# Kernel optimization log

Hardware: AMD Instinct MI355X
Metric: run time of the kernel (lower is better)

## Reference

```python
import jax, jax.numpy as jnp
import numpy as np

DIM = 192
HEADS = 6
WS = (6, 12)          # (lat, lon) window
INPUT_SHAPE = (186, 360)
TOW = INPUT_SHAPE[0] // WS[0]   # 31 latitude window types
N_WIN = WS[0] * WS[1]           # 72 tokens per window


def _position_index():
    """Earth-specific relative-position index (static, numpy)."""
    ws0, ws1 = WS
    coords_hi = np.arange(ws0)
    coords_hj = -np.arange(ws0) * ws0
    coords_w = np.arange(ws1)
    c1 = np.stack(np.meshgrid(coords_hi, coords_w, indexing='ij'))  # (2, ws0, ws1)
    c2 = np.stack(np.meshgrid(coords_hj, coords_w, indexing='ij'))
    f1 = c1.reshape(2, -1)
    f2 = c2.reshape(2, -1)
    coords = f1[:, :, None] - f2[:, None, :]      # (2, N, N)
    coords = coords.transpose(1, 2, 0).copy()     # (N, N, 2)
    coords[:, :, 1] += ws1 - 1                    # shift lon diff to >= 0
    coords[:, :, 0] *= 2 * ws1 - 1                # row stride in bias table
    return jnp.asarray(coords.sum(-1).reshape(-1))  # (N*N,) int


def setup_inputs() -> dict:
    key = jax.random.key(0)
    ks = jax.random.split(key, 6)
    B = 2
    nW = INPUT_SHAPE[1] // WS[1]          # 30
    B_ = B * TOW * nW                     # 1860
    table_rows = (2 * WS[1] - 1) * WS[0] * WS[0]  # 828
    return {
        "x": jax.random.normal(ks[0], (B_, N_WIN, DIM), dtype=jnp.float32),
        "mask": jnp.zeros((nW, N_WIN, N_WIN), dtype=jnp.float32),
        "w_qkv": jax.random.normal(ks[1], (DIM, 3 * DIM), dtype=jnp.float32) * 0.02,
        "b_qkv": jnp.zeros((3 * DIM,), dtype=jnp.float32),
        "w_out": jax.random.normal(ks[2], (DIM, DIM), dtype=jnp.float32) * 0.02,
        "b_out": jnp.zeros((DIM,), dtype=jnp.float32),
        "bias_table": jax.random.normal(ks[3], (table_rows, TOW, HEADS), dtype=jnp.float32) * 0.02,
    }


def reference(x, mask, w_qkv, b_qkv, w_out, b_out, bias_table):
    B_, N, dim = x.shape
    hd = dim // HEADS
    scale = hd ** -0.5
    # fused QKV projection
    qkv = (x @ w_qkv + b_qkv).reshape(B_, N, 3, HEADS, hd)
    qkv = qkv.transpose(2, 0, 3, 1, 4)            # (3, B_, H, N, hd)
    q, k, v = qkv[0] * scale, qkv[1], qkv[2]
    attn = jnp.einsum('bhnd,bhmd->bhnm', q, k)    # (B_, H, N, N)
    # earth-specific bias: gather table rows by relative-position index,
    # tiled across the window batch exactly as the torch code's .repeat()
    rep = B_ // TOW
    pos = _position_index()                       # (N*N,)
    bias = bias_table[jnp.tile(pos, rep)]         # (rep*N*N, TOW, H)
    bias = bias.reshape(N, N, -1, HEADS).transpose(2, 3, 0, 1)  # (B_, H, N, N)
    attn = attn + bias
    # window mask (broadcast over groups of nW lon-windows)
    nW = mask.shape[0]
    attn = attn.reshape(B_ // nW, nW, HEADS, N, N) + mask[None, :, None]
    attn = attn.reshape(B_, HEADS, N, N)
    attn = jax.nn.softmax(attn, axis=-1)          # dropout is identity (p=0 / eval)
    out = jnp.einsum('bhnm,bhmd->bhnd', attn, v)  # (B_, H, N, hd)
    out = out.transpose(0, 2, 1, 3).reshape(B_, N, dim)
    return out @ w_out + b_out
```

## Files before the change

### kernel.cpp

```cpp
#include <hip/hip_runtime.h>
#include <cstddef>

typedef short bf16x8 __attribute__((ext_vector_type(8)));
typedef float f32x4  __attribute__((ext_vector_type(4)));

namespace {
constexpr float QSCALE = 0.17677669529663687f;

constexpr size_t BQKV_OFF = 0;
constexpr size_t WOUT_OFF = 576 * 384 * 2;
constexpr size_t BQG_OFF  = WOUT_OFF + 192 * 384 * 2;
constexpr size_t QG_OFF   = BQG_OFF + 576 * 4;
constexpr size_t KG_OFF   = QG_OFF + (size_t)11160 * 2304 * 2;
constexpr size_t VG_OFF   = KG_OFF + (size_t)11160 * 2304 * 2;

constexpr int AXS = 392;
}

__device__ __forceinline__ unsigned short f2bf(float f) {
  unsigned int u = __builtin_bit_cast(unsigned int, f);
  return (unsigned short)((u + 0x7FFFu + ((u >> 16) & 1u)) >> 16);
}
__device__ __forceinline__ float bf2f(unsigned short h) {
  unsigned int u = ((unsigned int)h) << 16;
  return __builtin_bit_cast(float, u);
}
__device__ __forceinline__ int moffv(int i) { return (i < 4) ? i * 16 : 56; }

__global__ __launch_bounds__(256)
void prep_kernel(const float* __restrict__ wqkv, const float* __restrict__ bqkv,
                 const float* __restrict__ wout, unsigned char* __restrict__ ws) {
  int t = blockIdx.x * 256 + threadIdx.x;
  unsigned short* Bq = (unsigned short*)(ws + BQKV_OFF);
  unsigned short* Bo = (unsigned short*)(ws + WOUT_OFF);
  float* bqg = (float*)(ws + BQG_OFF);
  if (t < 576 * 384) {
    int n = t / 384, kk = t % 384;
    int ksrc = kk % 192, part = kk / 192;
    int h = n / 96, r96 = n % 96, kind = r96 / 32, d = r96 % 32;
    float w = wqkv[(size_t)ksrc * 576 + kind * 192 + h * 32 + d];
    if (kind == 0) w *= QSCALE;
    unsigned short hi = f2bf(w);
    Bq[t] = part ? f2bf(w - bf2f(hi)) : hi;
  } else if (t < 576 * 384 + 192 * 384) {
    int t2 = t - 576 * 384;
    int n = t2 / 384, kk = t2 % 384, ksrc = kk % 192, part = kk / 192;
    float w = wout[(size_t)ksrc * 192 + n];
    unsigned short hi = f2bf(w);
    Bo[t2] = part ? f2bf(w - bf2f(hi)) : hi;
  } else if (t < 576 * 384 + 192 * 384 + 576) {
    int n = t - (576 * 384 + 192 * 384);
    int h = n / 96, r96 = n % 96, kind = r96 / 32, d = r96 % 32;
    float b = bqkv[kind * 192 + h * 32 + d];
    if (kind == 0) b *= QSCALE;
    bqg[n] = b;
  }
}

template<int NM>
__device__ __forceinline__ void split_gemm(const unsigned short* __restrict__ sm,
                                           const unsigned short* __restrict__ Bt,
                                           int ngb, int m0idx, int lanen, int quad,
                                           f32x4 (&acc)[3][NM]) {
  #pragma unroll
  for (int nt = 0; nt < 3; ++nt)
    #pragma unroll
    for (int mi = 0; mi < NM; ++mi)
      acc[nt][mi] = (f32x4){0.f, 0.f, 0.f, 0.f};
  #pragma unroll 1
  for (int reg = 0; reg < 3; ++reg) {
    const int ab = (reg == 2) ? 192 : 0;
    const int bb = (reg == 1) ? 192 : 0;
    #pragma unroll 2
    for (int s = 0; s < 6; ++s) {
      bf16x8 a[NM];
      #pragma unroll
      for (int mi = 0; mi < NM; ++mi)
        a[mi] = *(const bf16x8*)(sm + (moffv(m0idx + mi) + lanen) * AXS + ab + 32 * s + quad * 8);
      #pragma unroll
      for (int nt = 0; nt < 3; ++nt) {
        bf16x8 bfr = *(const bf16x8*)(Bt + (size_t)((ngb + nt) * 16 + lanen) * 384 + bb + 32 * s + quad * 8);
        #pragma unroll
        for (int mi = 0; mi < NM; ++mi)
          acc[nt][mi] = __builtin_amdgcn_mfma_f32_16x16x32_bf16(a[mi], bfr, acc[nt][mi], 0, 0, 0);
      }
    }
  }
}

template<int NM>
__device__ __forceinline__ void qkv_epi(const f32x4 (&acc)[3][NM], const float* __restrict__ bqg,
                                        unsigned short* __restrict__ qg, unsigned short* __restrict__ kg,
                                        unsigned short* __restrict__ vg,
                                        int w, int ngb, int m0idx, int lanen, int quad) {
  #pragma unroll 1
  for (int nt = 0; nt < 3; ++nt) {
    const int ng = ngb + nt;
    const int h = ng / 6, w6 = (ng % 6) * 16;
    const float bias = bqg[ng * 16 + lanen];
    const size_t base = (size_t)(w * 6 + h) * 2304;
    #pragma unroll
    for (int mi = 0; mi < NM; ++mi) {
      const int mo = moffv(m0idx + mi);
      if (w6 < 64) {
        unsigned short* dst = ((w6 < 32) ? qg : kg) + base + (w6 & 31) + lanen;
        #pragma unroll
        for (int r = 0; r < 4; ++r)
          dst[(size_t)(mo + quad * 4 + r) * 32] = f2bf(acc[nt][mi][r] + bias);
      } else {
        const int d = (w6 - 64) + lanen;
        ushort4 hv;
        hv.x = f2bf(acc[nt][mi][0] + bias); hv.y = f2bf(acc[nt][mi][1] + bias);
        hv.z = f2bf(acc[nt][mi][2] + bias); hv.w = f2bf(acc[nt][mi][3] + bias);
        *(ushort4*)(vg + base + (size_t)d * 72 + mo + quad * 4) = hv;
      }
    }
  }
}

__global__ __launch_bounds__(512)
void qkv_kernel(const float* __restrict__ x, unsigned char* __restrict__ ws) {
  __shared__ unsigned short sm[72 * AXS];
  const int w = blockIdx.x, tid = threadIdx.x;
  const int lane = tid & 63, ty = tid >> 6;
  const int lanen = lane & 15, quad = lane >> 4;
  const float* xw = x + (size_t)w * (72 * 192);

  for (int i = tid; i < 3456; i += 512) {
    int r = i / 48, c4 = i % 48;
    float4 v = *(const float4*)(xw + r * 192 + c4 * 4);
    unsigned short h0 = f2bf(v.x), h1 = f2bf(v.y), h2 = f2bf(v.z), h3 = f2bf(v.w);
    ushort4 hv; hv.x = h0; hv.y = h1; hv.z = h2; hv.w = h3;
    ushort4 lv;
    lv.x = f2bf(v.x - bf2f(h0)); lv.y = f2bf(v.y - bf2f(h1));
    lv.z = f2bf(v.z - bf2f(h2)); lv.w = f2bf(v.w - bf2f(h3));
    *(ushort4*)(sm + r * AXS + c4 * 4) = hv;
    *(ushort4*)(sm + r * AXS + 192 + c4 * 4) = lv;
  }
  __syncthreads();

  const unsigned short* Bq = (const unsigned short*)(ws + BQKV_OFF);
  const float* bqg = (const float*)(ws + BQG_OFF);
  unsigned short* qg = (unsigned short*)(ws + QG_OFF);
  unsigned short* kg = (unsigned short*)(ws + KG_OFF);
  unsigned short* vg = (unsigned short*)(ws + VG_OFF);

  const int mg = ty >> 2, nq = ty & 3;
  #pragma unroll 1
  for (int it = 0; it < 3; ++it) {
    const int ngb = (nq + 4 * it) * 3;
    if (mg == 0) {
      f32x4 acc[3][3];
      split_gemm<3>(sm, Bq, ngb, 0, lanen, quad, acc);
      qkv_epi<3>(acc, bqg, qg, kg, vg, w, ngb, 0, lanen, quad);
    } else {
      f32x4 acc[3][2];
      split_gemm<2>(sm, Bq, ngb, 3, lanen, quad, acc);
      qkv_epi<2>(acc, bqg, qg, kg, vg, w, ngb, 3, lanen, quad);
    }
  }
}

__global__ __launch_bounds__(320)
void attn_core(const float* __restrict__ mask, const float* __restrict__ btab,
               const unsigned char* __restrict__ ws, float* __restrict__ out) {
  __shared__ unsigned short V2[32 * 104];
  __shared__ unsigned short PB[5 * 16 * 104];
  const int b = blockIdx.x, w = b / 6, hh = b - w * 6;
  const int tid = threadIdx.x, lane = tid & 63, ty = tid >> 6;
  const int lanen = lane & 15, quad = lane >> 4;
  const int mrow = w % 30, tlat = w % 31, w31 = w / 31;
  const unsigned short* qg = (const unsigned short*)(ws + QG_OFF) + (size_t)b * 2304;
  const unsigned short* kg = (const unsigned short*)(ws + KG_OFF) + (size_t)b * 2304;
  const unsigned short* vg = (const unsigned short*)(ws + VG_OFF) + (size_t)b * 2304;
  const float* maskw = mask + (size_t)mrow * 5184;

  for (int i = tid; i < 416; i += 320) {
    int r = i / 13, c = i - r * 13;
    uint4 z = make_uint4(0u, 0u, 0u, 0u);
    *(uint4*)(V2 + r * 104 + c * 8) = (c < 9) ? *(const uint4*)(vg + r * 72 + c * 8) : z;
  }
  {
    int wv = tid >> 6, rr = (tid >> 2) & 15, c = tid & 3;
    *(uint4*)(PB + wv * 1664 + rr * 104 + 72 + c * 8) = make_uint4(0u, 0u, 0u, 0u);
  }
  __syncthreads();

  const int mo = moffv(ty);
  unsigned short* pb = PB + ty * 1664;

  bf16x8 afr = *(const bf16x8*)(qg + (mo + lanen) * 32 + quad * 8);
  f32x4 s[5];
  #pragma unroll
  for (int t = 0; t < 5; ++t) {
    int no = (t < 4) ? t * 16 : 64;
    bf16x8 bfr = *(const bf16x8*)(kg + (no + lanen) * 32 + quad * 8);
    s[t] = (f32x4){0.f, 0.f, 0.f, 0.f};
    s[t] = __builtin_amdgcn_mfma_f32_16x16x32_bf16(afr, bfr, s[t], 0, 0, 0);
  }
  float lg[5][4];
  #pragma unroll
  for (int t = 0; t < 5; ++t) {
    int ct = ((t < 4) ? t * 16 : 64) + lanen;
    #pragma unroll
    for (int r = 0; r < 4; ++r) {
      if (ct < 72) {
        int m = mo + quad * 4 + r;
        unsigned int e = (unsigned)(m % 6); e = e ? 6u - e : 0u;
        unsigned int T = 864u * e + 60u * (unsigned)ct + (unsigned)w31;
        if (T >= 5184u) T -= 5184u;
        unsigned int p1 = T / 72u, p2 = T - 72u * p1;
        unsigned int i1 = p1 / 12u, j1 = p1 - 12u * i1;
        unsigned int i2 = p2 / 12u, j2 = p2 - 12u * i2;
        int rowb = (int)((i1 + 6u * i2) * 23u + j1) - (int)j2 + 11;
        float bv = btab[(size_t)rowb * 186 + tlat * 6 + hh];
        lg[t][r] = s[t][r] + bv + maskw[m * 72 + ct];
      } else lg[t][r] = -1e30f;
    }
  }
  #pragma unroll
  for (int r = 0; r < 4; ++r) {
    float mx = fmaxf(fmaxf(fmaxf(lg[0][r], lg[1][r]), fmaxf(lg[2][r], lg[3][r])), lg[4][r]);
    #pragma unroll
    for (int o = 8; o > 0; o >>= 1) mx = fmaxf(mx, __shfl_xor(mx, o));
    float sum = 0.f;
    #pragma unroll
    for (int t = 0; t < 5; ++t) { lg[t][r] = __expf(lg[t][r] - mx); sum += lg[t][r]; }
    #pragma unroll
    for (int o = 8; o > 0; o >>= 1) sum += __shfl_xor(sum, o);
    float inv = 1.0f / sum;
    #pragma unroll
    for (int t = 0; t < 5; ++t) {
      int ct = ((t < 4) ? t * 16 : 64) + lanen;
      if (ct < 72) pb[(quad * 4 + r) * 104 + ct] = f2bf(lg[t][r] * inv);
    }
  }
  f32x4 o2[2];
  o2[0] = (f32x4){0.f, 0.f, 0.f, 0.f}; o2[1] = (f32x4){0.f, 0.f, 0.f, 0.f};
  #pragma unroll
  for (int ks = 0; ks < 3; ++ks) {
    bf16x8 pfr = *(const bf16x8*)(pb + lanen * 104 + ks * 32 + quad * 8);
    #pragma unroll
    for (int n2 = 0; n2 < 2; ++n2) {
      bf16x8 vfr = *(const bf16x8*)(V2 + (n2 * 16 + lanen) * 104 + ks * 32 + quad * 8);
      o2[n2] = __builtin_amdgcn_mfma_f32_16x16x32_bf16(pfr, vfr, o2[n2], 0, 0, 0);
    }
  }
  #pragma unroll
  for (int n2 = 0; n2 < 2; ++n2) {
    int col = hh * 32 + n2 * 16 + lanen;
    #pragma unroll
    for (int r = 0; r < 4; ++r)
      out[((size_t)w * 72 + mo + quad * 4 + r) * 192 + col] = o2[n2][r];
  }
}

__global__ __launch_bounds__(512)
void outproj_kernel(const unsigned char* __restrict__ ws, const float* __restrict__ bout,
                    float* __restrict__ out) {
  __shared__ unsigned short Ax[72 * AXS];
  const int w = blockIdx.x, tid = threadIdx.x;
  const int lane = tid & 63, ty = tid >> 6;
  const int lanen = lane & 15, quad = lane >> 4;
  const unsigned short* Bo = (const unsigned short*)(ws + WOUT_OFF);
  float* rows = out + (size_t)w * (72 * 192);

  for (int i = tid; i < 3456; i += 512) {
    int r = i / 48, c4 = i % 48;
    float4 v = *(const float4*)(rows + r * 192 + c4 * 4);
    unsigned short h0 = f2bf(v.x), h1 = f2bf(v.y), h2 = f2bf(v.z), h3 = f2bf(v.w);
    ushort4 hv; hv.x = h0; hv.y = h1; hv.z = h2; hv.w = h3;
    ushort4 lv;
    lv.x = f2bf(v.x - bf2f(h0)); lv.y = f2bf(v.y - bf2f(h1));
    lv.z = f2bf(v.z - bf2f(h2)); lv.w = f2bf(v.w - bf2f(h3));
    *(ushort4*)(Ax + r * AXS + c4 * 4) = hv;
    *(ushort4*)(Ax + r * AXS + 192 + c4 * 4) = lv;
  }
  __syncthreads();

  const int mg = ty >> 2, nq = ty & 3;
  const int ngb = nq * 3;
  if (mg == 0) {
    f32x4 acc[3][3];
    split_gemm<3>(Ax, Bo, ngb, 0, lanen, quad, acc);
    #pragma unroll 1
    for (int nt = 0; nt < 3; ++nt) {
      const int n16 = (ngb + nt) * 16;
      const float bias = bout[n16 + lanen];
      #pragma unroll
      for (int mi = 0; mi < 3; ++mi) {
        const int mo = moffv(mi);
        #pragma unroll
        for (int r = 0; r < 4; ++r)
          rows[(size_t)(mo + quad * 4 + r) * 192 + n16 + lanen] = acc[nt][mi][r] + bias;
      }
    }
  } else {
    f32x4 acc[3][2];
    split_gemm<2>(Ax, Bo, ngb, 3, lanen, quad, acc);
    #pragma unroll 1
    for (int nt = 0; nt < 3; ++nt) {
      const int n16 = (ngb + nt) * 16;
      const float bias = bout[n16 + lanen];
      #pragma unroll
      for (int mi = 0; mi < 2; ++mi) {
        const int mo = moffv(3 + mi);
        #pragma unroll
        for (int r = 0; r < 4; ++r)
          rows[(size_t)(mo + quad * 4 + r) * 192 + n16 + lanen] = acc[nt][mi][r] + bias;
      }
    }
  }
}

extern "C" void kernel_launch(void* const* d_in, const int* in_sizes, int n_in,
                              void* d_out, int out_size, void* d_ws, size_t ws_size,
                              hipStream_t stream) {
  const float* x    = (const float*)d_in[0];
  const float* mask = (const float*)d_in[1];
  const float* wqkv = (const float*)d_in[2];
  const float* bqkv = (const float*)d_in[3];
  const float* wout = (const float*)d_in[4];
  const float* bout = (const float*)d_in[5];
  const float* btab = (const float*)d_in[6];
  float* out = (float*)d_out;
  unsigned char* ws = (unsigned char*)d_ws;
  const int nwindows = in_sizes[0] / (72 * 192);

  prep_kernel<<<dim3(1155), dim3(256), 0, stream>>>(wqkv, bqkv, wout, ws);
  qkv_kernel<<<dim3(nwindows), dim3(512), 0, stream>>>(x, ws);
  attn_core<<<dim3(nwindows * 6), dim3(320), 0, stream>>>(mask, btab, ws, out);
  outproj_kernel<<<dim3(nwindows), dim3(512), 0, stream>>>(ws, bout, out);
}
```

Measured before the change: 864.7 us.

## Software-pipeline split GEMM loads, store V row-major, and overlap attention prologue

The split-bf16 GEMM loop is fully unrolled and double-buffers the A and B fragments, so the loads for step t+1 are issued before the MFMAs of step t. The QKV epilogue now writes V in the same row-major layout as Q and K, and attn_core transposes V into shared memory itself. attn_core also computes the bias and mask terms and stages V while the QK^T MFMAs are pending, and moves the block barrier to just before the PV product. waves_per_eu hints are added to all three kernels, which trades register budget for occupancy and may cause spills.

Result: slower. 1.089 ms (+25.9%).

```diff
diff --git a/kernel.cpp b/kernel.cpp
--- a/kernel.cpp
+++ b/kernel.cpp
@@ -62,29 +62,45 @@
                                            const unsigned short* __restrict__ Bt,
                                            int ngb, int m0idx, int lanen, int quad,
                                            f32x4 (&acc)[3][NM]) {
+  const unsigned short* arow[NM];
+  #pragma unroll
+  for (int mi = 0; mi < NM; ++mi)
+    arow[mi] = sm + (moffv(m0idx + mi) + lanen) * AXS + quad * 8;
+  const unsigned short* brow[3];
+  #pragma unroll
+  for (int nt = 0; nt < 3; ++nt)
+    brow[nt] = Bt + (size_t)((ngb + nt) * 16 + lanen) * 384 + quad * 8;
+
   #pragma unroll
   for (int nt = 0; nt < 3; ++nt)
     #pragma unroll
     for (int mi = 0; mi < NM; ++mi)
       acc[nt][mi] = (f32x4){0.f, 0.f, 0.f, 0.f};
-  #pragma unroll 1
-  for (int reg = 0; reg < 3; ++reg) {
-    const int ab = (reg == 2) ? 192 : 0;
-    const int bb = (reg == 1) ? 192 : 0;
-    #pragma unroll 2
-    for (int s = 0; s < 6; ++s) {
-      bf16x8 a[NM];
+
+  bf16x8 aB[2][NM], bB[2][3];
+  #pragma unroll
+  for (int mi = 0; mi < NM; ++mi) aB[0][mi] = *(const bf16x8*)(arow[mi]);
+  #pragma unroll
+  for (int nt = 0; nt < 3; ++nt)  bB[0][nt] = *(const bf16x8*)(brow[nt]);
+
+  #pragma unroll
+  for (int t = 0; t < 18; ++t) {
+    const int cur = t & 1, nxt = cur ^ 1;
+    if (t < 17) {
+      const int t1 = t + 1, reg1 = t1 / 6, s1 = t1 % 6;
+      const int ab1 = (reg1 == 2) ? 192 : 0, bb1 = (reg1 == 1) ? 192 : 0;
       #pragma unroll
       for (int mi = 0; mi < NM; ++mi)
-        a[mi] = *(const bf16x8*)(sm + (moffv(m0idx + mi) + lanen) * AXS + ab + 32 * s + quad * 8);
-      #pragma unroll
-      for (int nt = 0; nt < 3; ++nt) {
-        bf16x8 bfr = *(const bf16x8*)(Bt + (size_t)((ngb + nt) * 16 + lanen) * 384 + bb + 32 * s + quad * 8);
-        #pragma unroll
-        for (int mi = 0; mi < NM; ++mi)
-          acc[nt][mi] = __builtin_amdgcn_mfma_f32_16x16x32_bf16(a[mi], bfr, acc[nt][mi], 0, 0, 0);
-      }
-    }
+        aB[nxt][mi] = *(const bf16x8*)(arow[mi] + ab1 + 32 * s1);
+      #pragma unroll
+      for (int nt = 0; nt < 3; ++nt)
+        bB[nxt][nt] = *(const bf16x8*)(brow[nt] + bb1 + 32 * s1);
+    }
+    #pragma unroll
+    for (int nt = 0; nt < 3; ++nt)
+      #pragma unroll
+      for (int mi = 0; mi < NM; ++mi)
+        acc[nt][mi] = __builtin_amdgcn_mfma_f32_16x16x32_bf16(aB[cur][mi], bB[cur][nt], acc[nt][mi], 0, 0, 0);
   }
 }
 
@@ -97,28 +113,22 @@
   for (int nt = 0; nt < 3; ++nt) {
     const int ng = ngb + nt;
     const int h = ng / 6, w6 = (ng % 6) * 16;
+    const int kind = w6 >> 5, cb = w6 & 31;
     const float bias = bqg[ng * 16 + lanen];
     const size_t base = (size_t)(w * 6 + h) * 2304;
+    unsigned short* dst = ((kind == 0) ? qg : (kind == 1) ? kg : vg) + base + cb + lanen;
     #pragma unroll
     for (int mi = 0; mi < NM; ++mi) {
       const int mo = moffv(m0idx + mi);
-      if (w6 < 64) {
-        unsigned short* dst = ((w6 < 32) ? qg : kg) + base + (w6 & 31) + lanen;
-        #pragma unroll
-        for (int r = 0; r < 4; ++r)
-          dst[(size_t)(mo + quad * 4 + r) * 32] = f2bf(acc[nt][mi][r] + bias);
-      } else {
-        const int d = (w6 - 64) + lanen;
-        ushort4 hv;
-        hv.x = f2bf(acc[nt][mi][0] + bias); hv.y = f2bf(acc[nt][mi][1] + bias);
-        hv.z = f2bf(acc[nt][mi][2] + bias); hv.w = f2bf(acc[nt][mi][3] + bias);
-        *(ushort4*)(vg + base + (size_t)d * 72 + mo + quad * 4) = hv;
-      }
+      #pragma unroll
+      for (int r = 0; r < 4; ++r)
+        dst[(size_t)(mo + quad * 4 + r) * 32] = f2bf(acc[nt][mi][r] + bias);
     }
   }
 }
 
 __global__ __launch_bounds__(512)
+__attribute__((amdgpu_waves_per_eu(4, 4)))
 void qkv_kernel(const float* __restrict__ x, unsigned char* __restrict__ ws) {
   __shared__ unsigned short sm[72 * AXS];
   const int w = blockIdx.x, tid = threadIdx.x;
@@ -162,6 +172,7 @@
 }
 
 __global__ __launch_bounds__(320)
+__attribute__((amdgpu_waves_per_eu(4, 4)))
 void attn_core(const float* __restrict__ mask, const float* __restrict__ btab,
                const unsigned char* __restrict__ ws, float* __restrict__ out) {
   __shared__ unsigned short V2[32 * 104];
@@ -175,30 +186,16 @@
   const unsigned short* vg = (const unsigned short*)(ws + VG_OFF) + (size_t)b * 2304;
   const float* maskw = mask + (size_t)mrow * 5184;
 
-  for (int i = tid; i < 416; i += 320) {
-    int r = i / 13, c = i - r * 13;
-    uint4 z = make_uint4(0u, 0u, 0u, 0u);
-    *(uint4*)(V2 + r * 104 + c * 8) = (c < 9) ? *(const uint4*)(vg + r * 72 + c * 8) : z;
-  }
-  {
-    int wv = tid >> 6, rr = (tid >> 2) & 15, c = tid & 3;
-    *(uint4*)(PB + wv * 1664 + rr * 104 + 72 + c * 8) = make_uint4(0u, 0u, 0u, 0u);
-  }
-  __syncthreads();
-
   const int mo = moffv(ty);
-  unsigned short* pb = PB + ty * 1664;
 
   bf16x8 afr = *(const bf16x8*)(qg + (mo + lanen) * 32 + quad * 8);
-  f32x4 s[5];
+  bf16x8 kfr[5];
   #pragma unroll
   for (int t = 0; t < 5; ++t) {
     int no = (t < 4) ? t * 16 : 64;
-    bf16x8 bfr = *(const bf16x8*)(kg + (no + lanen) * 32 + quad * 8);
-    s[t] = (f32x4){0.f, 0.f, 0.f, 0.f};
-    s[t] = __builtin_amdgcn_mfma_f32_16x16x32_bf16(afr, bfr, s[t], 0, 0, 0);
-  }
-  float lg[5][4];
+    kfr[t] = *(const bf16x8*)(kg + (no + lanen) * 32 + quad * 8);
+  }
+  float pre[5][4];
   #pragma unroll
   for (int t = 0; t < 5; ++t) {
     int ct = ((t < 4) ? t * 16 : 64) + lanen;
@@ -213,10 +210,41 @@
         unsigned int i1 = p1 / 12u, j1 = p1 - 12u * i1;
         unsigned int i2 = p2 / 12u, j2 = p2 - 12u * i2;
         int rowb = (int)((i1 + 6u * i2) * 23u + j1) - (int)j2 + 11;
-        float bv = btab[(size_t)rowb * 186 + tlat * 6 + hh];
-        lg[t][r] = s[t][r] + bv + maskw[m * 72 + ct];
-      } else lg[t][r] = -1e30f;
-    }
+        pre[t][r] = btab[(size_t)rowb * 186 + tlat * 6 + hh] + maskw[m * 72 + ct];
+      } else pre[t][r] = 0.f;
+    }
+  }
+
+  for (int i = tid; i < 576; i += 320) {
+    int t = i >> 3, c = i & 7;
+    ushort4 vv = *(const ushort4*)(vg + t * 32 + c * 4);
+    V2[(c * 4 + 0) * 104 + t] = vv.x; V2[(c * 4 + 1) * 104 + t] = vv.y;
+    V2[(c * 4 + 2) * 104 + t] = vv.z; V2[(c * 4 + 3) * 104 + t] = vv.w;
+  }
+  for (int i = tid; i < 1024; i += 320) {
+    int d = i >> 5, j = i & 31;
+    V2[d * 104 + 72 + j] = 0;
+  }
+  {
+    int wv = tid >> 6, rr = (tid >> 2) & 15, c = tid & 3;
+    *(uint4*)(PB + wv * 1664 + rr * 104 + 72 + c * 8) = make_uint4(0u, 0u, 0u, 0u);
+  }
+
+  f32x4 s[5];
+  #pragma unroll
+  for (int t = 0; t < 5; ++t) {
+    s[t] = (f32x4){0.f, 0.f, 0.f, 0.f};
+    s[t] = __builtin_amdgcn_mfma_f32_16x16x32_bf16(afr, kfr[t], s[t], 0, 0, 0);
+  }
+
+  unsigned short* pb = PB + ty * 1664;
+  float lg[5][4];
+  #pragma unroll
+  for (int t = 0; t < 5; ++t) {
+    int ct = ((t < 4) ? t * 16 : 64) + lanen;
+    #pragma unroll
+    for (int r = 0; r < 4; ++r)
+      lg[t][r] = (ct < 72) ? (s[t][r] + pre[t][r]) : -1e30f;
   }
   #pragma unroll
   for (int r = 0; r < 4; ++r) {
@@ -235,6 +263,9 @@
       if (ct < 72) pb[(quad * 4 + r) * 104 + ct] = f2bf(lg[t][r] * inv);
     }
   }
+
+  __syncthreads();
+
   f32x4 o2[2];
   o2[0] = (f32x4){0.f, 0.f, 0.f, 0.f}; o2[1] = (f32x4){0.f, 0.f, 0.f, 0.f};
   #pragma unroll
@@ -256,6 +287,7 @@
 }
 
 __global__ __launch_bounds__(512)
+__attribute__((amdgpu_waves_per_eu(4, 4)))
 void outproj_kernel(const unsigned char* __restrict__ ws, const float* __restrict__ bout,
                     float* __restrict__ out) {
   __shared__ unsigned short Ax[72 * AXS];
```
